# Kernel tuning notes

Hardware: AMD Instinct MI355X
Metric: run time of the kernel (lower is better)

Reference implementation:

```python
import jax, jax.numpy as jnp
import numpy as np

PROPOSAL_COUNT = 100
IOU_THRESHOLD = 0.3
SCORE_THRESHOLD = 0.7
MEAN = np.array([0.0, 0.0, 0.0, 0.0], np.float32)
STD = np.array([0.1, 0.1, 0.2, 0.2], np.float32)
CLIP_RATIO = 16.0 / 1000.0
NEG = -1e9  # finite -inf sentinel (avoids NaNs)


def delta2bbox(anchors, delta):
    # anchors: (..., 4) xyxy, delta: (..., 4) normalized dx,dy,dw,dh
    delta = delta * STD + MEAN
    w = anchors[..., 2] - anchors[..., 0]
    h = anchors[..., 3] - anchors[..., 1]
    cx = anchors[..., 0] + 0.5 * w
    cy = anchors[..., 1] + 0.5 * h
    max_ratio = abs(float(np.log(CLIP_RATIO)))
    dx, dy = delta[..., 0], delta[..., 1]
    dw = jnp.clip(delta[..., 2], -max_ratio, max_ratio)
    dh = jnp.clip(delta[..., 3], -max_ratio, max_ratio)
    pcx = cx + dx * w
    pcy = cy + dy * h
    pw = w * jnp.exp(dw)
    ph = h * jnp.exp(dh)
    return jnp.stack([pcx - 0.5 * pw, pcy - 0.5 * ph, pcx + 0.5 * pw, pcy + 0.5 * ph], axis=-1)


def iou_one(box, boxes):
    # box: (4,), boxes: (N, 4) -> (N,)
    ix1 = jnp.maximum(box[0], boxes[..., 0])
    iy1 = jnp.maximum(box[1], boxes[..., 1])
    ix2 = jnp.minimum(box[2], boxes[..., 2])
    iy2 = jnp.minimum(box[3], boxes[..., 3])
    inter = jnp.maximum(ix2 - ix1, 0.0) * jnp.maximum(iy2 - iy1, 0.0)
    area1 = (box[2] - box[0]) * (box[3] - box[1])
    area2 = (boxes[..., 2] - boxes[..., 0]) * (boxes[..., 3] - boxes[..., 1])
    return inter / jnp.maximum(area1 + area2 - inter, 1e-9)


def greedy_nms(scores, boxes):
    # masked greedy hard-NMS with fixed PROPOSAL_COUNT iterations
    # scores: (N,) with NEG on invalid entries, boxes: (N, 4)
    def step(s, _):
        i = jnp.argmax(s)
        si = s[i]
        sel = si > 0.5 * NEG
        iou = iou_one(boxes[i], boxes)
        s = jnp.where(sel & (iou > IOU_THRESHOLD), NEG, s)
        s = s.at[i].set(NEG)
        return s, (jnp.where(sel, i, -1), jnp.where(sel, si, NEG))
    _, (idx, sc) = jax.lax.scan(step, scores, None, length=PROPOSAL_COUNT)
    return idx, sc  # (P,), (P,)


def filter_detection(logits, regress, anchors):
    B, N, C = logits.shape
    # decode + clip (elementwise, same math as gathering first then decoding)
    boxes = jnp.clip(delta2bbox(anchors[None], regress), 0.0, 1.0)  # (B,N,4)
    label = jnp.argmax(logits, axis=-1)                             # (B,N)
    fg = label > 0                                                  # background filter
    scores = jnp.moveaxis(logits[..., 1:], -1, 1)                   # (B,C-1,N)
    valid = fg[:, None, :] & (scores >= SCORE_THRESHOLD)
    s0 = jnp.where(valid, scores, NEG)
    # selection indices are piecewise constant in the inputs
    s0_c = jax.lax.stop_gradient(s0)
    boxes_c = jax.lax.stop_gradient(boxes)
    nms_b = jax.vmap(jax.vmap(greedy_nms, in_axes=(0, None)), in_axes=(0, 0))
    sel_idx, sel_sc = nms_b(s0_c, boxes_c)                          # (B,C-1,P)
    K = (C - 1) * PROPOSAL_COUNT
    idx_flat = sel_idx.reshape(B, K)
    sc_flat = sel_sc.reshape(B, K)
    # global top-k over all classes, sorted descending (matches tf.nn.top_k)
    top_sc, top_pos = jax.lax.top_k(sc_flat, PROPOSAL_COUNT)        # (B,P)
    anchor_idx = jnp.take_along_axis(idx_flat, top_pos, axis=1)
    ok = (top_sc > 0.5 * NEG)[..., None].astype(logits.dtype)       # padding mask
    safe = jnp.maximum(anchor_idx, 0)
    out_logit = jnp.take_along_axis(logits, safe[..., None], axis=1) * ok  # (B,P,C)
    out_box = jnp.take_along_axis(boxes, safe[..., None], axis=1) * ok     # (B,P,4)
    return out_logit, out_box


def setup_inputs() -> dict:
    key = jax.random.key(0)
    k1, k2, k3, k4 = jax.random.split(key, 4)
    B, N, C = 4, 100000, 41
    logits = jax.random.normal(k1, (B, N, C), jnp.float32)
    regress = jax.random.normal(k2, (B, N, 4), jnp.float32) * 0.5
    xy = jax.random.uniform(k3, (N, 2), jnp.float32) * 0.8
    wh = jax.random.uniform(k4, (N, 2), jnp.float32) * 0.2 + 0.01
    anchors = jnp.concatenate([xy, jnp.minimum(xy + wh, 1.0)], axis=-1)  # valid xyxy in [0,1]
    return {"logits": logits, "regress": regress, "anchors": anchors}


def reference(logits, regress, anchors):
    return filter_detection(logits, regress, anchors)
```

## Files before the change

kernel.cpp:

```cpp
#include <hip/hip_runtime.h>
#include <cstdint>
#include <cstddef>

#define BN 4
#define NN 100000
#define CC 41
#define NCLS 40
#define NPROB (BN * NCLS)
#define PROP 100
#define NEGV (-1e9f)
#define IOU_T 0.3f
#define SCORE_T 0.7f
#define MAXR 4.135166556742356f
#define CAP 2048
#define TARGET 512
#define LISTCAP 26624
#define NBMPW 3125
#define E07 0xBF333333u
#define ERHI 0xC1800000u
#define W0 ((unsigned long long)(ERHI - E07))
#define NT3 1024
#define CHK 8192
#define NCHKB 4

__device__ __forceinline__ unsigned int encf(float x) {
  unsigned int u = __float_as_uint(x);
  return (u & 0x80000000u) ? ~u : (u | 0x80000000u);
}
__device__ __forceinline__ float decf(unsigned int e) {
  unsigned int u = (e & 0x80000000u) ? (e ^ 0x80000000u) : ~e;
  return __uint_as_float(u);
}

__device__ __forceinline__ float iou_f(float ax1, float ay1, float ax2, float ay2,
                                       float bx1, float by1, float bx2, float by2) {
  float ix1 = fmaxf(ax1, bx1), iy1 = fmaxf(ay1, by1);
  float ix2 = fminf(ax2, bx2), iy2 = fminf(ay2, by2);
  float inter = fmaxf(ix2 - ix1, 0.0f) * fmaxf(iy2 - iy1, 0.0f);
  float a1 = (ax2 - ax1) * (ay2 - ay1);
  float a2 = (bx2 - bx1) * (by2 - by1);
  return inter / fmaxf(a1 + a2 - inter, 1e-9f);
}

__device__ __forceinline__ int select_window(const unsigned int* h, int* lo_out) {
  unsigned int cum = 0; int lo = 256; int act = 2;
  for (int bb = 255; bb >= 0; --bb) {
    unsigned int nb = h[bb];
    if (nb == 0u) continue;
    if (cum + nb > CAP) {
      if (cum == 0u) { act = 1; }
      break;
    }
    cum += nb; lo = bb; act = 0;
    if (cum >= TARGET) break;
  }
  *lo_out = lo;
  return act;
}

__global__ void decode_kernel(const float4* __restrict__ regress,
                              const float4* __restrict__ anchors,
                              float4* __restrict__ boxes,
                              unsigned int* __restrict__ gcnt,
                              unsigned int* __restrict__ ghist) {
  int i = blockIdx.x * 256 + threadIdx.x;
  if (i < NPROB) gcnt[i] = 0u;
  if (i < NPROB * 256) ghist[i] = 0u;
  if (i >= BN * NN) return;
  int n = i % NN;
  float4 d = regress[i];
  float4 a = anchors[n];
  float w = a.z - a.x, h = a.w - a.y;
  float cx = a.x + 0.5f * w, cy = a.y + 0.5f * h;
  float dx = d.x * 0.1f, dy = d.y * 0.1f;
  float dw = fminf(fmaxf(d.z * 0.2f, -MAXR), MAXR);
  float dh = fminf(fmaxf(d.w * 0.2f, -MAXR), MAXR);
  float pcx = cx + dx * w, pcy = cy + dy * h;
  float pw = w * expf(dw), ph = h * expf(dh);
  float4 o;
  o.x = fminf(fmaxf(pcx - 0.5f * pw, 0.0f), 1.0f);
  o.y = fminf(fmaxf(pcy - 0.5f * ph, 0.0f), 1.0f);
  o.z = fminf(fmaxf(pcx + 0.5f * pw, 0.0f), 1.0f);
  o.w = fminf(fmaxf(pcy + 0.5f * ph, 0.0f), 1.0f);
  boxes[i] = o;
}

__global__ void score_kernel(const float* __restrict__ logits,
                             unsigned long long* __restrict__ glist,
                             unsigned int* __restrict__ gcnt,
                             unsigned int* __restrict__ fgb) {
  __shared__ float lg[256 * CC];
  __shared__ unsigned short wpre[NCLS][4];
  __shared__ unsigned int cbase[NCLS];
  int b = blockIdx.y;
  int n0 = blockIdx.x * 256;
  int tid = threadIdx.x;
  int wave = tid >> 6, lane = tid & 63;
  int rows = NN - n0; if (rows > 256) rows = 256;
  int total4 = rows * CC / 4;
  const float4* src = (const float4*)(logits + ((size_t)b * NN + n0) * CC);
  float4* dst = (float4*)lg;
  for (int i = tid; i < total4; i += 256) dst[i] = src[i];
  __syncthreads();

  bool act = tid < rows;
  int n = n0 + tid;
  float bestv = 0.0f; int bestc = 0;
  if (act) {
    bestv = lg[tid * CC];
    #pragma unroll
    for (int c = 1; c < CC; ++c) {
      float v = lg[tid * CC + c];
      if (v > bestv) { bestv = v; bestc = c; }
    }
  }
  bool fg = act && (bestc > 0);
  int wbase = n0 + (tid & ~63);

  unsigned long long mfg = __ballot(fg);
  if (lane == 0 && wbase < NN) fgb[b * NBMPW + (wbase >> 5)] = (unsigned int)mfg;
  if (lane == 32 && wbase + 32 < NN) fgb[b * NBMPW + (wbase >> 5) + 1] = (unsigned int)(mfg >> 32);

  #pragma unroll 4
  for (int c = 1; c < CC; ++c) {
    float v = act ? lg[tid * CC + c] : 0.0f;
    unsigned long long m = __ballot(fg && (v >= SCORE_T));
    if (lane == 0) wpre[c - 1][wave] = (unsigned short)__popcll(m);
  }
  __syncthreads();

  if (tid < NCLS) {
    unsigned int t0 = wpre[tid][0], t1 = wpre[tid][1], t2 = wpre[tid][2], t3 = wpre[tid][3];
    unsigned int tot = t0 + t1 + t2 + t3;
    unsigned int base = tot ? atomicAdd(&gcnt[b * NCLS + tid], tot) : 0u;
    cbase[tid] = base;
    wpre[tid][0] = 0;
    wpre[tid][1] = (unsigned short)t0;
    wpre[tid][2] = (unsigned short)(t0 + t1);
    wpre[tid][3] = (unsigned short)(t0 + t1 + t2);
  }
  __syncthreads();

  #pragma unroll 4
  for (int c = 1; c < CC; ++c) {
    float v = act ? lg[tid * CC + c] : 0.0f;
    bool elig = fg && (v >= SCORE_T);
    unsigned long long m = __ballot(elig);
    if (elig) {
      unsigned int pos = cbase[c - 1] + wpre[c - 1][wave]
                       + (unsigned int)__popcll(m & ((1ull << lane) - 1ull));
      if (pos < LISTCAP)
        glist[(size_t)(b * NCLS + (c - 1)) * LISTCAP + pos] =
            ((unsigned long long)encf(v) << 32) | (unsigned int)n;
    }
  }
}

__global__ void hist_kernel(const unsigned long long* __restrict__ glist,
                            const unsigned int* __restrict__ gcnt,
                            unsigned int* __restrict__ ghist) {
  __shared__ unsigned int h[256];
  int prob = blockIdx.y;
  int chunk = blockIdx.x;
  int tid = threadIdx.x;
  unsigned int cnt = gcnt[prob];
  if (cnt > LISTCAP) return;
  h[tid] = 0u;
  __syncthreads();
  unsigned int lo = chunk * CHK;
  unsigned int hi = cnt < lo + CHK ? cnt : lo + CHK;
  const unsigned long long* list = glist + (size_t)prob * LISTCAP;
  for (unsigned int i = lo + tid; i < hi; i += 256) {
    unsigned long long E = list[i] >> 32;
    unsigned int bin = (E >= ERHI) ? 255u : (unsigned int)(((E - E07) << 8) / W0);
    atomicAdd(&h[bin], 1u);
  }
  __syncthreads();
  unsigned int v = h[tid];
  if (v) atomicAdd(&ghist[prob * 256 + tid], v);
}

__device__ int sort_walk(int ncand, int nsel,
                         unsigned long long* keysL, float4* boxesL, float4* selL,
                         int* sh_nsel, int prob, int* __restrict__ oidx,
                         float* __restrict__ osc, int tid) {
  if (ncand == 0) return nsel;
  int M = 64; while (M < ncand) M <<= 1;
  for (int i = ncand + tid; i < M; i += NT3) keysL[i] = 0ull;
  __syncthreads();
  for (int k = 2; k <= M; k <<= 1) {
    for (int j = k >> 1; j > 0; j >>= 1) {
      for (int t = tid; t < M; t += NT3) {
        int ixj = t ^ j;
        if (ixj > t) {
          unsigned long long a = keysL[t], c2 = keysL[ixj];
          bool up = ((t & k) == 0);
          if (up ? (a < c2) : (a > c2)) { keysL[t] = c2; keysL[ixj] = a; }
        }
      }
      __syncthreads();
    }
  }
  if (tid < 64) {
    int lane = tid;
    int ns = nsel;
    for (int base = 0; base < ncand && ns < PROP; base += 64) {
      int i = base + lane;
      bool valid = i < ncand;
      unsigned long long key = valid ? keysL[i] : 0ull;
      int slot = (int)(key & 0x7FFF);
      float4 bx = boxesL[valid ? slot : 0];
      float sc = decf((unsigned int)(key >> 32));
      int aidx = 131071 - (int)((key >> 15) & 0x1FFFF);
      bool supp = false;
      for (int j = 0; j < ns; ++j) {
        float4 sb = selL[j];
        supp = supp || (iou_f(bx.x, bx.y, bx.z, bx.w, sb.x, sb.y, sb.z, sb.w) > IOU_T);
      }
      unsigned long long live = __ballot(valid && !supp);
      while (live && ns < PROP) {
        int kk = __ffsll(live) - 1;
        float x1 = __shfl(bx.x, kk), y1 = __shfl(bx.y, kk);
        float x2 = __shfl(bx.z, kk), y2 = __shfl(bx.w, kk);
        float ksc = __shfl(sc, kk);
        int kidx = __shfl(aidx, kk);
        if (lane == 0) {
          oidx[prob * PROP + ns] = kidx;
          osc [prob * PROP + ns] = ksc;
          selL[ns] = make_float4(x1, y1, x2, y2);
        }
        ns++;
        if (lane > kk && valid && !supp)
          supp = iou_f(bx.x, bx.y, bx.z, bx.w, x1, y1, x2, y2) > IOU_T;
        live = __ballot(valid && !supp) & ~((2ull << kk) - 1ull);
      }
    }
    if (lane == 0) *sh_nsel = ns;
  }
  __syncthreads();
  return *sh_nsel;
}

__device__ int process_window(unsigned long long WLO, unsigned long long WUP, int idxbin,
                              bool dense, unsigned int cnt,
                              const unsigned long long* list, const float* lcol,
                              const unsigned int* fgp, const float4* bx4,
                              unsigned long long* keysL, float4* boxesL, float4* selL,
                              int* sh_cnt, int* sh_nsel,
                              int nsel, int prob, int* __restrict__ oidx,
                              float* __restrict__ osc, int tid) {
  __syncthreads();
  if (tid == 0) *sh_cnt = 0;
  __syncthreads();
  if (!dense) {
    for (unsigned int i = tid; i < cnt; i += NT3) {
      unsigned long long k = list[i];
      unsigned long long E = k >> 32;
      unsigned int idx = (unsigned int)(k & 0xFFFFFFFFu);
      if (E >= WLO && E < WUP && (idxbin < 0 || (int)(idx >> 9) == idxbin)) {
        int slot = atomicAdd(sh_cnt, 1);
        if (slot < CAP) {
          keysL[slot] = (E << 32)
                      | ((unsigned long long)((131071u - idx) & 0x1FFFFu) << 15)
                      | (unsigned long long)slot;
          boxesL[slot] = bx4[idx];
        }
      }
    }
  } else {
    for (int i = tid; i < NN; i += NT3) {
      if (!((fgp[i >> 5] >> (i & 31)) & 1u)) continue;
      float s = lcol[(size_t)i * CC];
      if (s < SCORE_T) continue;
      unsigned long long E = encf(s);
      if (E >= WLO && E < WUP && (idxbin < 0 || (i >> 9) == idxbin)) {
        int slot = atomicAdd(sh_cnt, 1);
        if (slot < CAP) {
          keysL[slot] = (E << 32)
                      | ((unsigned long long)((131071u - (unsigned int)i) & 0x1FFFFu) << 15)
                      | (unsigned long long)slot;
          boxesL[slot] = bx4[i];
        }
      }
    }
  }
  __syncthreads();
  int ncand = *sh_cnt; if (ncand > CAP) ncand = CAP;
  return sort_walk(ncand, nsel, keysL, boxesL, selL, sh_nsel, prob, oidx, osc, tid);
}

__launch_bounds__(NT3)
__global__ void nms_finish(const unsigned long long* __restrict__ glist,
                           const unsigned int* __restrict__ gcnt,
                           const float* __restrict__ logits,
                           const unsigned int* __restrict__ fgb,
                           const float4* __restrict__ boxes,
                           const unsigned int* __restrict__ ghist,
                           int* __restrict__ oidx, float* __restrict__ osc) {
  __shared__ unsigned int hist[256];
  __shared__ unsigned long long keysL[CAP];
  __shared__ float4 boxesL[CAP];
  __shared__ float4 selL[PROP];
  __shared__ int sh_cnt, sh_nsel, sh_action, sh_bin;
  __shared__ unsigned int sh_wlo;

  int prob = blockIdx.x;
  int b = prob / NCLS;
  int c1 = prob % NCLS + 1;
  int tid = threadIdx.x;

  unsigned int cnt = gcnt[prob];
  bool dense = cnt > LISTCAP;
  const unsigned long long* list = glist + (size_t)prob * LISTCAP;
  const float4* bx4 = boxes + (size_t)b * NN;
  const float* lcol = logits + (size_t)b * NN * CC + c1;
  const unsigned int* fgp = fgb + b * NBMPW;

  unsigned long long EHI = 1ull << 32;
  int nsel = 0;

  if (tid == 0) {
    int act = 1;
    unsigned int wlo = 0;
    if (!dense) {
      int lo;
      act = select_window(&ghist[prob * 256], &lo);
      if (act == 0) wlo = E07 + (unsigned int)(((unsigned long long)lo * W0 + 255ull) >> 8);
    }
    sh_action = act; sh_wlo = wlo; sh_cnt = 0;
  }
  __syncthreads();

  if (sh_action == 0) {
    unsigned long long wlo = sh_wlo;
    for (unsigned int i = tid; i < cnt; i += NT3) {
      unsigned long long k = list[i];
      unsigned long long E = k >> 32;
      if (E >= wlo) {
        unsigned int idx = (unsigned int)(k & 0xFFFFFFFFu);
        int slot = atomicAdd(&sh_cnt, 1);
        if (slot < CAP) {
          keysL[slot] = (E << 32)
                      | ((unsigned long long)((131071u - idx) & 0x1FFFFu) << 15)
                      | (unsigned long long)slot;
          boxesL[slot] = bx4[idx];
        }
      }
    }
    __syncthreads();
    int ncand = sh_cnt < CAP ? sh_cnt : CAP;
    nsel = sort_walk(ncand, 0, keysL, boxesL, selL, &sh_nsel, prob, oidx, osc, tid);
    EHI = sh_wlo;
  }

  for (int round = 0; round < 200 && nsel < PROP; ++round) {
    unsigned long long Rlo = E07, Rhi = ERHI;
    int level = 0;
    int action;
    unsigned long long WLO = 0, WUP = 0, E0 = 0;
    bool idxmode = false;

    while (true) {
      if (tid < 256) hist[tid] = 0u;
      __syncthreads();
      unsigned long long up = (level == 0) ? EHI : (Rhi < EHI ? Rhi : EHI);
      unsigned long long W = (level == 0) ? W0 : (Rhi - Rlo);
      if (!dense) {
        for (unsigned int i = tid; i < cnt; i += NT3) {
          unsigned long long E = list[i] >> 32;
          if (E >= Rlo && E < up) {
            unsigned int bin = (level == 0 && E >= ERHI) ? 255u
                             : (unsigned int)(((E - Rlo) << 8) / W);
            atomicAdd(&hist[bin], 1u);
          }
        }
      } else {
        for (int i = tid; i < NN; i += NT3) {
          if (!((fgp[i >> 5] >> (i & 31)) & 1u)) continue;
          float s = lcol[(size_t)i * CC];
          if (s < SCORE_T) continue;
          unsigned long long E = encf(s);
          if (E >= Rlo && E < up) {
            unsigned int bin = (level == 0 && E >= ERHI) ? 255u
                             : (unsigned int)(((E - Rlo) << 8) / W);
            atomicAdd(&hist[bin], 1u);
          }
        }
      }
      __syncthreads();
      if (tid == 0) {
        int lo;
        int act = select_window(hist, &lo);
        int rb = -1;
        if (act == 1) {
          for (int bb = 255; bb >= 0; --bb) if (hist[bb]) { rb = bb; break; }
        }
        sh_action = act; sh_bin = (act == 1) ? rb : lo;
      }
      __syncthreads();
      action = sh_action;
      int bsel = sh_bin;
      if (action == 2) break;
      if (action == 0) {
        WLO = Rlo + (((unsigned long long)bsel * W + 255ull) >> 8);
        WUP = up;
        break;
      }
      unsigned long long nRlo = Rlo + (((unsigned long long)bsel * W + 255ull) >> 8);
      unsigned long long nRhi = (level == 0 && bsel == 255)
                                ? EHI
                                : Rlo + (((unsigned long long)(bsel + 1) * W + 255ull) >> 8);
      if (nRhi > EHI) nRhi = EHI;
      Rlo = nRlo; Rhi = nRhi; level = 1;
      if (Rhi - Rlo <= 1ull) { idxmode = true; E0 = Rlo; break; }
    }

    if (action == 2) break;

    if (!idxmode) {
      nsel = process_window(WLO, WUP, -1, dense, cnt, list, lcol, fgp, bx4,
                            keysL, boxesL, selL, &sh_cnt, &sh_nsel,
                            nsel, prob, oidx, osc, tid);
      EHI = WLO;
    } else {
      for (int ib = 0; ib < 256 && nsel < PROP; ++ib)
        nsel = process_window(E0, E0 + 1ull, ib, dense, cnt, list, lcol, fgp, bx4,
                              keysL, boxesL, selL, &sh_cnt, &sh_nsel,
                              nsel, prob, oidx, osc, tid);
      EHI = E0;
    }
  }

  __syncthreads();
  for (int p = nsel + tid; p < PROP; p += NT3) {
    oidx[prob * PROP + p] = -1;
    osc [prob * PROP + p] = NEGV;
  }
}

__global__ void topk_kernel(const float* __restrict__ logits,
                            const float4* __restrict__ boxes,
                            const int* __restrict__ oidx,
                            const float* __restrict__ osc,
                            float* __restrict__ out) {
  __shared__ unsigned long long keys[4096];
  int b = blockIdx.x;
  int tid = threadIdx.x;
  for (int i = tid; i < 4096; i += 1024) {
    unsigned long long key = 0ull;
    if (i < NCLS * PROP) {
      float sc = osc[b * NCLS * PROP + i];
      key = ((unsigned long long)encf(sc) << 32) | (unsigned int)(~i);
    }
    keys[i] = ~key;
  }
  __syncthreads();
  for (int k = 2; k <= 4096; k <<= 1) {
    for (int j = k >> 1; j > 0; j >>= 1) {
      for (int t = tid; t < 4096; t += 1024) {
        int ixj = t ^ j;
        if (ixj > t) {
          unsigned long long a = keys[t], c2 = keys[ixj];
          bool up = ((t & k) == 0);
          if ((a > c2) == up) { keys[t] = c2; keys[ixj] = a; }
        }
      }
      __syncthreads();
    }
  }
  if (tid < PROP) {
    unsigned long long key = ~keys[tid];
    unsigned int e = (unsigned int)(key >> 32);
    float sc = decf(e);
    bool ok = sc > 0.5f * NEGV;
    int kk = (int)(~(unsigned int)key);
    if (kk < 0 || kk >= NCLS * PROP) kk = 0;
    int idx = ok ? oidx[b * NCLS * PROP + kk] : 0;
    if (idx < 0) idx = 0;
    float m = ok ? 1.0f : 0.0f;
    const float* lp = logits + ((size_t)b * NN + idx) * CC;
    float* outl = out + ((size_t)b * PROP + tid) * CC;
    #pragma unroll
    for (int c = 0; c < CC; ++c) outl[c] = lp[c] * m;
    float4 bb = boxes[(size_t)b * NN + idx];
    float* outb = out + (size_t)BN * PROP * CC + ((size_t)b * PROP + tid) * 4;
    outb[0] = bb.x * m; outb[1] = bb.y * m; outb[2] = bb.z * m; outb[3] = bb.w * m;
  }
}

extern "C" void kernel_launch(void* const* d_in, const int* in_sizes, int n_in,
                              void* d_out, int out_size, void* d_ws, size_t ws_size,
                              hipStream_t stream) {
  const float* logits  = (const float*)d_in[0];
  const float* regress = (const float*)d_in[1];
  const float* anchors = (const float*)d_in[2];
  float* out = (float*)d_out;

  char* ws = (char*)d_ws;
  size_t off = 0;
  float4* boxes = (float4*)(ws + off);            off += (size_t)BN * NN * 16;
  unsigned long long* glist = (unsigned long long*)(ws + off); off += (size_t)NPROB * LISTCAP * 8;
  unsigned int* gcnt = (unsigned int*)(ws + off); off += NPROB * 4;
  unsigned int* fgb  = (unsigned int*)(ws + off); off += BN * NBMPW * 4;
  float* osc = (float*)(ws + off);                off += NPROB * PROP * 4;
  int*   oidx = (int*)(ws + off);                 off += NPROB * PROP * 4;
  unsigned int* ghist = (unsigned int*)(ws + off); off += NPROB * 256 * 4;

  decode_kernel<<<(BN * NN + 255) / 256, 256, 0, stream>>>(
      (const float4*)regress, (const float4*)anchors, boxes, gcnt, ghist);
  score_kernel<<<dim3((NN + 255) / 256, BN), 256, 0, stream>>>(logits, glist, gcnt, fgb);
  hist_kernel<<<dim3(NCHKB, NPROB), 256, 0, stream>>>(glist, gcnt, ghist);
  nms_finish<<<NPROB, NT3, 0, stream>>>(glist, gcnt, logits, fgb, boxes, ghist, oidx, osc);
  topk_kernel<<<BN, 1024, 0, stream>>>(logits, boxes, oidx, osc, out);
}
```

Before: 218.2 us.

## Use finer global histogram, wave-shuffle bitonic sort, and histogram-driven window walk

Raises the global score histogram from 256 to 1024 bins so the NMS block can repeatedly pick descending score windows from the precomputed histogram, with no per-round rebuild of a block-local histogram over the whole candidate list. The bitonic sort now handles strides below 64 with register shuffles in place of shared-memory passes and barriers. LISTCAP grows so more problems stay on the sparse list path. The cost is more histogram atomics and memory, plus a more intricate fallback path whose correctness depends on the bin-edge arithmetic.

```diff
diff --git a/kernel.cpp b/kernel.cpp
--- a/kernel.cpp
+++ b/kernel.cpp
@@ -14,7 +14,7 @@
 #define MAXR 4.135166556742356f
 #define CAP 2048
 #define TARGET 512
-#define LISTCAP 26624
+#define LISTCAP 32768
 #define NBMPW 3125
 #define E07 0xBF333333u
 #define ERHI 0xC1800000u
@@ -22,6 +22,9 @@
 #define NT3 1024
 #define CHK 8192
 #define NCHKB 4
+#define NB0 1024
+
+typedef unsigned long long ull;
 
 __device__ __forceinline__ unsigned int encf(float x) {
   unsigned int u = __float_as_uint(x);
@@ -30,6 +33,9 @@
 __device__ __forceinline__ float decf(unsigned int e) {
   unsigned int u = (e & 0x80000000u) ? (e ^ 0x80000000u) : ~e;
   return __uint_as_float(u);
+}
+__device__ __forceinline__ ull edge0(int bb) {
+  return (ull)E07 + (((ull)bb * W0 + (NB0 - 1)) >> 10);
 }
 
 __device__ __forceinline__ float iou_f(float ax1, float ay1, float ax2, float ay2,
@@ -42,13 +48,13 @@
   return inter / fmaxf(a1 + a2 - inter, 1e-9f);
 }
 
-__device__ __forceinline__ int select_window(const unsigned int* h, int* lo_out) {
-  unsigned int cum = 0; int lo = 256; int act = 2;
-  for (int bb = 255; bb >= 0; --bb) {
+__device__ __forceinline__ int select_window_h(const unsigned int* h, int hibin, int* lo_out) {
+  unsigned int cum = 0; int lo = hibin; int act = 2;
+  for (int bb = hibin - 1; bb >= 0; --bb) {
     unsigned int nb = h[bb];
     if (nb == 0u) continue;
     if (cum + nb > CAP) {
-      if (cum == 0u) { act = 1; }
+      if (cum == 0u) { act = 1; lo = bb; }
       break;
     }
     cum += nb; lo = bb; act = 0;
@@ -65,7 +71,7 @@
                               unsigned int* __restrict__ ghist) {
   int i = blockIdx.x * 256 + threadIdx.x;
   if (i < NPROB) gcnt[i] = 0u;
-  if (i < NPROB * 256) ghist[i] = 0u;
+  if (i < NPROB * NB0) ghist[i] = 0u;
   if (i >= BN * NN) return;
   int n = i % NN;
   float4 d = regress[i];
@@ -86,7 +92,7 @@
 }
 
 __global__ void score_kernel(const float* __restrict__ logits,
-                             unsigned long long* __restrict__ glist,
+                             ull* __restrict__ glist,
                              unsigned int* __restrict__ gcnt,
                              unsigned int* __restrict__ fgb) {
   __shared__ float lg[256 * CC];
@@ -151,63 +157,94 @@
                        + (unsigned int)__popcll(m & ((1ull << lane) - 1ull));
       if (pos < LISTCAP)
         glist[(size_t)(b * NCLS + (c - 1)) * LISTCAP + pos] =
-            ((unsigned long long)encf(v) << 32) | (unsigned int)n;
-    }
-  }
-}
-
-__global__ void hist_kernel(const unsigned long long* __restrict__ glist,
+            ((ull)encf(v) << 32) | (unsigned int)n;
+    }
+  }
+}
+
+__global__ void hist_kernel(const ull* __restrict__ glist,
                             const unsigned int* __restrict__ gcnt,
                             unsigned int* __restrict__ ghist) {
-  __shared__ unsigned int h[256];
+  __shared__ unsigned int h[NB0];
   int prob = blockIdx.y;
   int chunk = blockIdx.x;
   int tid = threadIdx.x;
   unsigned int cnt = gcnt[prob];
   if (cnt > LISTCAP) return;
-  h[tid] = 0u;
+  for (int i = tid; i < NB0; i += 256) h[i] = 0u;
   __syncthreads();
   unsigned int lo = chunk * CHK;
   unsigned int hi = cnt < lo + CHK ? cnt : lo + CHK;
-  const unsigned long long* list = glist + (size_t)prob * LISTCAP;
+  const ull* list = glist + (size_t)prob * LISTCAP;
   for (unsigned int i = lo + tid; i < hi; i += 256) {
-    unsigned long long E = list[i] >> 32;
-    unsigned int bin = (E >= ERHI) ? 255u : (unsigned int)(((E - E07) << 8) / W0);
+    ull E = list[i] >> 32;
+    unsigned int bin = (E >= (ull)ERHI) ? (NB0 - 1)
+                     : (unsigned int)(((E - E07) << 10) / W0);
     atomicAdd(&h[bin], 1u);
   }
   __syncthreads();
-  unsigned int v = h[tid];
-  if (v) atomicAdd(&ghist[prob * 256 + tid], v);
-}
-
-__device__ int sort_walk(int ncand, int nsel,
-                         unsigned long long* keysL, float4* boxesL, float4* selL,
-                         int* sh_nsel, int prob, int* __restrict__ oidx,
-                         float* __restrict__ osc, int tid) {
-  if (ncand == 0) return nsel;
-  int M = 64; while (M < ncand) M <<= 1;
-  for (int i = ncand + tid; i < M; i += NT3) keysL[i] = 0ull;
-  __syncthreads();
-  for (int k = 2; k <= M; k <<= 1) {
+  for (int i = tid; i < NB0; i += 256) {
+    unsigned int v = h[i];
+    if (v) atomicAdd(&ghist[prob * NB0 + i], v);
+  }
+}
+
+__device__ __forceinline__ ull bswap_cmp(ull v, int e, int j, int k) {
+  ull p = __shfl_xor(v, j);
+  bool up = ((e & k) == 0);
+  bool low = ((e & j) == 0);
+  return (up == low) ? (v > p ? v : p) : (v < p ? v : p);
+}
+
+__device__ void bitonic_sort_desc(ull* keysL, int M, int tid) {
+  int e0 = tid, e1 = tid + 1024;
+  bool h0 = e0 < M, h1 = e1 < M;
+  ull v0 = h0 ? keysL[e0] : 0ull;
+  ull v1 = h1 ? keysL[e1] : 0ull;
+  for (int k = 2; k <= 64; k <<= 1) {
+    if (k > M) break;
     for (int j = k >> 1; j > 0; j >>= 1) {
+      if (h0) v0 = bswap_cmp(v0, e0, j, k);
+      if (h1) v1 = bswap_cmp(v1, e1, j, k);
+    }
+  }
+  if (h0) keysL[e0] = v0;
+  if (h1) keysL[e1] = v1;
+  __syncthreads();
+  for (int k = 128; k <= M; k <<= 1) {
+    for (int j = k >> 1; j >= 64; j >>= 1) {
       for (int t = tid; t < M; t += NT3) {
         int ixj = t ^ j;
         if (ixj > t) {
-          unsigned long long a = keysL[t], c2 = keysL[ixj];
+          ull a = keysL[t], c2 = keysL[ixj];
           bool up = ((t & k) == 0);
           if (up ? (a < c2) : (a > c2)) { keysL[t] = c2; keysL[ixj] = a; }
         }
       }
       __syncthreads();
     }
-  }
+    if (h0) v0 = keysL[e0];
+    if (h1) v1 = keysL[e1];
+    for (int j = 32; j > 0; j >>= 1) {
+      if (h0) v0 = bswap_cmp(v0, e0, j, k);
+      if (h1) v1 = bswap_cmp(v1, e1, j, k);
+    }
+    if (h0) keysL[e0] = v0;
+    if (h1) keysL[e1] = v1;
+    __syncthreads();
+  }
+}
+
+__device__ int walk(int ncand, int nsel, const ull* keysL, const float4* boxesL,
+                    float4* selL, int* sh_nsel, int prob,
+                    int* __restrict__ oidx, float* __restrict__ osc, int tid) {
   if (tid < 64) {
     int lane = tid;
     int ns = nsel;
     for (int base = 0; base < ncand && ns < PROP; base += 64) {
       int i = base + lane;
       bool valid = i < ncand;
-      unsigned long long key = valid ? keysL[i] : 0ull;
+      ull key = valid ? keysL[i] : 0ull;
       int slot = (int)(key & 0x7FFF);
       float4 bx = boxesL[valid ? slot : 0];
       float sc = decf((unsigned int)(key >> 32));
@@ -241,28 +278,28 @@
   return *sh_nsel;
 }
 
-__device__ int process_window(unsigned long long WLO, unsigned long long WUP, int idxbin,
-                              bool dense, unsigned int cnt,
-                              const unsigned long long* list, const float* lcol,
-                              const unsigned int* fgp, const float4* bx4,
-                              unsigned long long* keysL, float4* boxesL, float4* selL,
-                              int* sh_cnt, int* sh_nsel,
-                              int nsel, int prob, int* __restrict__ oidx,
-                              float* __restrict__ osc, int tid) {
+__device__ int compact_sort_walk(ull WLO, ull WUP, int idxbin,
+                                 bool dense, unsigned int cnt,
+                                 const ull* list, const float* lcol,
+                                 const unsigned int* fgp, const float4* bx4,
+                                 ull* keysL, float4* boxesL, float4* selL,
+                                 int* sh_cnt, int* sh_nsel,
+                                 int nsel, int prob, int* __restrict__ oidx,
+                                 float* __restrict__ osc, int tid) {
   __syncthreads();
   if (tid == 0) *sh_cnt = 0;
   __syncthreads();
   if (!dense) {
     for (unsigned int i = tid; i < cnt; i += NT3) {
-      unsigned long long k = list[i];
-      unsigned long long E = k >> 32;
+      ull k = list[i];
+      ull E = k >> 32;
       unsigned int idx = (unsigned int)(k & 0xFFFFFFFFu);
       if (E >= WLO && E < WUP && (idxbin < 0 || (int)(idx >> 9) == idxbin)) {
         int slot = atomicAdd(sh_cnt, 1);
         if (slot < CAP) {
           keysL[slot] = (E << 32)
-                      | ((unsigned long long)((131071u - idx) & 0x1FFFFu) << 15)
-                      | (unsigned long long)slot;
+                      | ((ull)((131071u - idx) & 0x1FFFFu) << 15)
+                      | (ull)slot;
           boxesL[slot] = bx4[idx];
         }
       }
@@ -272,13 +309,13 @@
       if (!((fgp[i >> 5] >> (i & 31)) & 1u)) continue;
       float s = lcol[(size_t)i * CC];
       if (s < SCORE_T) continue;
-      unsigned long long E = encf(s);
+      ull E = encf(s);
       if (E >= WLO && E < WUP && (idxbin < 0 || (i >> 9) == idxbin)) {
         int slot = atomicAdd(sh_cnt, 1);
         if (slot < CAP) {
           keysL[slot] = (E << 32)
-                      | ((unsigned long long)((131071u - (unsigned int)i) & 0x1FFFFu) << 15)
-                      | (unsigned long long)slot;
+                      | ((ull)((131071u - (unsigned int)i) & 0x1FFFFu) << 15)
+                      | (ull)slot;
           boxesL[slot] = bx4[i];
         }
       }
@@ -286,23 +323,101 @@
   }
   __syncthreads();
   int ncand = *sh_cnt; if (ncand > CAP) ncand = CAP;
-  return sort_walk(ncand, nsel, keysL, boxesL, selL, sh_nsel, prob, oidx, osc, tid);
+  if (ncand == 0) return nsel;
+  int M = 64; while (M < ncand) M <<= 1;
+  for (int i = ncand + tid; i < M; i += NT3) keysL[i] = 0ull;
+  __syncthreads();
+  bitonic_sort_desc(keysL, M, tid);
+  return walk(ncand, nsel, keysL, boxesL, selL, sh_nsel, prob, oidx, osc, tid);
+}
+
+__device__ int fallback_range(ull Rlo0, ull Rhi0,
+                              bool dense, unsigned int cnt,
+                              const ull* list, const float* lcol,
+                              const unsigned int* fgp, const float4* bx4,
+                              ull* keysL, float4* boxesL, float4* selL,
+                              unsigned int* subh,
+                              int* sh_cnt, int* sh_nsel, int* sh_a, int* sh_b,
+                              int nsel, int prob, int* __restrict__ oidx,
+                              float* __restrict__ osc, int tid) {
+  ull EHIl = Rhi0;
+  for (int round = 0; round < 300 && nsel < PROP; ++round) {
+    ull Rlo = Rlo0, Rhi = EHIl;
+    int action; int bsel;
+    ull WLO = 0, WUP = 0, E0 = 0;
+    bool idxm = false;
+    while (true) {
+      for (int i = tid; i < 256; i += NT3) subh[i] = 0u;
+      __syncthreads();
+      ull W = Rhi - Rlo;
+      if (!dense) {
+        for (unsigned int i = tid; i < cnt; i += NT3) {
+          ull E = list[i] >> 32;
+          if (E >= Rlo && E < Rhi)
+            atomicAdd(&subh[(unsigned int)(((E - Rlo) << 8) / W)], 1u);
+        }
+      } else {
+        for (int i = tid; i < NN; i += NT3) {
+          if (!((fgp[i >> 5] >> (i & 31)) & 1u)) continue;
+          float s = lcol[(size_t)i * CC];
+          if (s < SCORE_T) continue;
+          ull E = encf(s);
+          if (E >= Rlo && E < Rhi)
+            atomicAdd(&subh[(unsigned int)(((E - Rlo) << 8) / W)], 1u);
+        }
+      }
+      __syncthreads();
+      if (tid == 0) {
+        int lo;
+        int act = select_window_h(subh, 256, &lo);
+        *sh_a = act; *sh_b = lo;
+      }
+      __syncthreads();
+      action = *sh_a; bsel = *sh_b;
+      __syncthreads();
+      if (action == 2) break;
+      if (action == 0) {
+        WLO = Rlo + (((ull)bsel * W + 255ull) >> 8);
+        WUP = Rhi;
+        break;
+      }
+      ull nRlo = Rlo + (((ull)bsel * W + 255ull) >> 8);
+      ull nRhi = Rlo + (((ull)(bsel + 1) * W + 255ull) >> 8);
+      if (nRhi > Rhi) nRhi = Rhi;
+      Rlo = nRlo; Rhi = nRhi;
+      if (Rhi - Rlo <= 1ull) { idxm = true; E0 = Rlo; break; }
+    }
+    if (action == 2) break;
+    if (!idxm) {
+      nsel = compact_sort_walk(WLO, WUP, -1, dense, cnt, list, lcol, fgp, bx4,
+                               keysL, boxesL, selL, sh_cnt, sh_nsel,
+                               nsel, prob, oidx, osc, tid);
+      EHIl = WLO;
+    } else {
+      for (int ib = 0; ib < 256 && nsel < PROP; ++ib)
+        nsel = compact_sort_walk(E0, E0 + 1ull, ib, dense, cnt, list, lcol, fgp, bx4,
+                                 keysL, boxesL, selL, sh_cnt, sh_nsel,
+                                 nsel, prob, oidx, osc, tid);
+      EHIl = E0;
+    }
+  }
+  return nsel;
 }
 
 __launch_bounds__(NT3)
-__global__ void nms_finish(const unsigned long long* __restrict__ glist,
+__global__ void nms_finish(const ull* __restrict__ glist,
                            const unsigned int* __restrict__ gcnt,
                            const float* __restrict__ logits,
                            const unsigned int* __restrict__ fgb,
                            const float4* __restrict__ boxes,
                            const unsigned int* __restrict__ ghist,
                            int* __restrict__ oidx, float* __restrict__ osc) {
-  __shared__ unsigned int hist[256];
-  __shared__ unsigned long long keysL[CAP];
+  __shared__ unsigned int histL[NB0];
+  __shared__ unsigned int subh[256];
+  __shared__ ull keysL[CAP];
   __shared__ float4 boxesL[CAP];
   __shared__ float4 selL[PROP];
-  __shared__ int sh_cnt, sh_nsel, sh_action, sh_bin;
-  __shared__ unsigned int sh_wlo;
+  __shared__ int sh_cnt, sh_nsel, sh_a, sh_b;
 
   int prob = blockIdx.x;
   int b = prob / NCLS;
@@ -311,123 +426,46 @@
 
   unsigned int cnt = gcnt[prob];
   bool dense = cnt > LISTCAP;
-  const unsigned long long* list = glist + (size_t)prob * LISTCAP;
+  const ull* list = glist + (size_t)prob * LISTCAP;
   const float4* bx4 = boxes + (size_t)b * NN;
   const float* lcol = logits + (size_t)b * NN * CC + c1;
   const unsigned int* fgp = fgb + b * NBMPW;
 
-  unsigned long long EHI = 1ull << 32;
   int nsel = 0;
 
-  if (tid == 0) {
-    int act = 1;
-    unsigned int wlo = 0;
-    if (!dense) {
-      int lo;
-      act = select_window(&ghist[prob * 256], &lo);
-      if (act == 0) wlo = E07 + (unsigned int)(((unsigned long long)lo * W0 + 255ull) >> 8);
-    }
-    sh_action = act; sh_wlo = wlo; sh_cnt = 0;
-  }
-  __syncthreads();
-
-  if (sh_action == 0) {
-    unsigned long long wlo = sh_wlo;
-    for (unsigned int i = tid; i < cnt; i += NT3) {
-      unsigned long long k = list[i];
-      unsigned long long E = k >> 32;
-      if (E >= wlo) {
-        unsigned int idx = (unsigned int)(k & 0xFFFFFFFFu);
-        int slot = atomicAdd(&sh_cnt, 1);
-        if (slot < CAP) {
-          keysL[slot] = (E << 32)
-                      | ((unsigned long long)((131071u - idx) & 0x1FFFFu) << 15)
-                      | (unsigned long long)slot;
-          boxesL[slot] = bx4[idx];
-        }
-      }
-    }
+  if (dense) {
+    nsel = fallback_range(E07, 1ull << 32, true, cnt, list, lcol, fgp, bx4,
+                          keysL, boxesL, selL, subh, &sh_cnt, &sh_nsel, &sh_a, &sh_b,
+                          0, prob, oidx, osc, tid);
+  } else {
+    for (int i = tid; i < NB0; i += NT3) histL[i] = ghist[prob * NB0 + i];
     __syncthreads();
-    int ncand = sh_cnt < CAP ? sh_cnt : CAP;
-    nsel = sort_walk(ncand, 0, keysL, boxesL, selL, &sh_nsel, prob, oidx, osc, tid);
-    EHI = sh_wlo;
-  }
-
-  for (int round = 0; round < 200 && nsel < PROP; ++round) {
-    unsigned long long Rlo = E07, Rhi = ERHI;
-    int level = 0;
-    int action;
-    unsigned long long WLO = 0, WUP = 0, E0 = 0;
-    bool idxmode = false;
-
-    while (true) {
-      if (tid < 256) hist[tid] = 0u;
-      __syncthreads();
-      unsigned long long up = (level == 0) ? EHI : (Rhi < EHI ? Rhi : EHI);
-      unsigned long long W = (level == 0) ? W0 : (Rhi - Rlo);
-      if (!dense) {
-        for (unsigned int i = tid; i < cnt; i += NT3) {
-          unsigned long long E = list[i] >> 32;
-          if (E >= Rlo && E < up) {
-            unsigned int bin = (level == 0 && E >= ERHI) ? 255u
-                             : (unsigned int)(((E - Rlo) << 8) / W);
-            atomicAdd(&hist[bin], 1u);
-          }
-        }
-      } else {
-        for (int i = tid; i < NN; i += NT3) {
-          if (!((fgp[i >> 5] >> (i & 31)) & 1u)) continue;
-          float s = lcol[(size_t)i * CC];
-          if (s < SCORE_T) continue;
-          unsigned long long E = encf(s);
-          if (E >= Rlo && E < up) {
-            unsigned int bin = (level == 0 && E >= ERHI) ? 255u
-                             : (unsigned int)(((E - Rlo) << 8) / W);
-            atomicAdd(&hist[bin], 1u);
-          }
-        }
-      }
-      __syncthreads();
+    int hibin = NB0;
+    while (nsel < PROP && hibin > 0) {
       if (tid == 0) {
         int lo;
-        int act = select_window(hist, &lo);
-        int rb = -1;
-        if (act == 1) {
-          for (int bb = 255; bb >= 0; --bb) if (hist[bb]) { rb = bb; break; }
-        }
-        sh_action = act; sh_bin = (act == 1) ? rb : lo;
-      }
-      __syncthreads();
-      action = sh_action;
-      int bsel = sh_bin;
-      if (action == 2) break;
-      if (action == 0) {
-        WLO = Rlo + (((unsigned long long)bsel * W + 255ull) >> 8);
-        WUP = up;
-        break;
-      }
-      unsigned long long nRlo = Rlo + (((unsigned long long)bsel * W + 255ull) >> 8);
-      unsigned long long nRhi = (level == 0 && bsel == 255)
-                                ? EHI
-                                : Rlo + (((unsigned long long)(bsel + 1) * W + 255ull) >> 8);
-      if (nRhi > EHI) nRhi = EHI;
-      Rlo = nRlo; Rhi = nRhi; level = 1;
-      if (Rhi - Rlo <= 1ull) { idxmode = true; E0 = Rlo; break; }
-    }
-
-    if (action == 2) break;
-
-    if (!idxmode) {
-      nsel = process_window(WLO, WUP, -1, dense, cnt, list, lcol, fgp, bx4,
-                            keysL, boxesL, selL, &sh_cnt, &sh_nsel,
-                            nsel, prob, oidx, osc, tid);
-      EHI = WLO;
-    } else {
-      for (int ib = 0; ib < 256 && nsel < PROP; ++ib)
-        nsel = process_window(E0, E0 + 1ull, ib, dense, cnt, list, lcol, fgp, bx4,
-                              keysL, boxesL, selL, &sh_cnt, &sh_nsel,
+        int act = select_window_h(histL, hibin, &lo);
+        sh_a = act; sh_b = lo;
+      }
+      __syncthreads();
+      int act = sh_a, bsel = sh_b;
+      __syncthreads();
+      if (act == 2) break;
+      if (act == 0) {
+        ull WLO = edge0(bsel);
+        ull WUP = (hibin == NB0) ? (1ull << 32) : edge0(hibin);
+        nsel = compact_sort_walk(WLO, WUP, -1, false, cnt, list, lcol, fgp, bx4,
+                                 keysL, boxesL, selL, &sh_cnt, &sh_nsel,
+                                 nsel, prob, oidx, osc, tid);
+        hibin = bsel;
+      } else {
+        ull Rlo = edge0(bsel);
+        ull Rhi = (bsel == NB0 - 1) ? (1ull << 32) : edge0(bsel + 1);
+        nsel = fallback_range(Rlo, Rhi, false, cnt, list, lcol, fgp, bx4,
+                              keysL, boxesL, selL, subh, &sh_cnt, &sh_nsel, &sh_a, &sh_b,
                               nsel, prob, oidx, osc, tid);
-      EHI = E0;
+        hibin = bsel;
+      }
     }
   }
 
@@ -443,14 +481,14 @@
                             const int* __restrict__ oidx,
                             const float* __restrict__ osc,
                             float* __restrict__ out) {
-  __shared__ unsigned long long keys[4096];
+  __shared__ ull keys[4096];
   int b = blockIdx.x;
   int tid = threadIdx.x;
   for (int i = tid; i < 4096; i += 1024) {
-    unsigned long long key = 0ull;
+    ull key = 0ull;
     if (i < NCLS * PROP) {
       float sc = osc[b * NCLS * PROP + i];
-      key = ((unsigned long long)encf(sc) << 32) | (unsigned int)(~i);
+      key = ((ull)encf(sc) << 32) | (unsigned int)(~i);
     }
     keys[i] = ~key;
   }
@@ -460,7 +498,7 @@
       for (int t = tid; t < 4096; t += 1024) {
         int ixj = t ^ j;
         if (ixj > t) {
-          unsigned long long a = keys[t], c2 = keys[ixj];
+          ull a = keys[t], c2 = keys[ixj];
           bool up = ((t & k) == 0);
           if ((a > c2) == up) { keys[t] = c2; keys[ixj] = a; }
         }
@@ -469,7 +507,7 @@
     }
   }
   if (tid < PROP) {
-    unsigned long long key = ~keys[tid];
+    ull key = ~keys[tid];
     unsigned int e = (unsigned int)(key >> 32);
     float sc = decf(e);
     bool ok = sc > 0.5f * NEGV;
@@ -499,12 +537,12 @@
   char* ws = (char*)d_ws;
   size_t off = 0;
   float4* boxes = (float4*)(ws + off);            off += (size_t)BN * NN * 16;
-  unsigned long long* glist = (unsigned long long*)(ws + off); off += (size_t)NPROB * LISTCAP * 8;
+  ull* glist = (ull*)(ws + off);                  off += (size_t)NPROB * LISTCAP * 8;
   unsigned int* gcnt = (unsigned int*)(ws + off); off += NPROB * 4;
   unsigned int* fgb  = (unsigned int*)(ws + off); off += BN * NBMPW * 4;
   float* osc = (float*)(ws + off);                off += NPROB * PROP * 4;
   int*   oidx = (int*)(ws + off);                 off += NPROB * PROP * 4;
-  unsigned int* ghist = (unsigned int*)(ws + off); off += NPROB * 256 * 4;
+  unsigned int* ghist = (unsigned int*)(ws + off); off += (size_t)NPROB * NB0 * 4;
 
   decode_kernel<<<(BN * NN + 255) / 256, 256, 0, stream>>>(
       (const float4*)regress, (const float4*)anchors, boxes, gcnt, ghist);
```

Result: slower. 265.6 us (+21.7%).
